# Kernel optimization log

Hardware: AMD Instinct MI355X
Metric: run time of the kernel (lower is better)

Reference implementation:

```python
import jax, jax.numpy as jnp
import numpy as np
from jax import lax

T, B, H, L = 512, 64, 512, 2  # seq_len, batch, hidden(=input), num_layers


def setup_inputs() -> dict:
    key = jax.random.key(0)
    ks = jax.random.split(key, 6)
    s = 1.0 / np.sqrt(H)  # torch default init scale
    x = jax.random.normal(ks[0], (T, B, H), dtype=jnp.float32)
    h0 = jax.random.normal(ks[1], (L, B, H), dtype=jnp.float32)
    W_ih = jax.random.uniform(ks[2], (L, H, H), jnp.float32, -s, s)
    W_hh = jax.random.uniform(ks[3], (L, H, H), jnp.float32, -s, s)
    b_ih = jax.random.uniform(ks[4], (L, H), jnp.float32, -s, s)
    b_hh = jax.random.uniform(ks[5], (L, H), jnp.float32, -s, s)
    return {"x": x, "h0": h0, "W_ih": W_ih, "W_hh": W_hh, "b_ih": b_ih, "b_hh": b_hh}


def _run_layer(x, h0, Wi, Wh, bi, bh):
    # Precompute input contribution for all timesteps: [T,B,H]
    xw = jnp.einsum('tbi,hi->tbh', x, Wi) + bi

    def step(h, xw_t):
        h_new = jnp.tanh(xw_t + h @ Wh.T + bh)
        return h_new, h_new

    h_last, ys = lax.scan(step, h0, xw)
    return ys, h_last


def reference(x, h0, W_ih, W_hh, b_ih, b_hh):
    # Multi-layer Elman RNN with tanh, matching torch.nn.RNN (batch_first=False).
    h_n = []
    out = x
    for l in range(L):
        out, h_last = _run_layer(out, h0[l], W_ih[l], W_hh[l], b_ih[l], b_hh[l])
        h_n.append(h_last)
    return out, jnp.stack(h_n, axis=0)
```

## Files before the change

kernel.cpp:

```cpp
#include <hip/hip_runtime.h>
#include <stdint.h>

#define T_ 512
#define B_ 64
#define H_ 512
#define L_ 2
#define TBH (T_*B_*H_)
#define BH  (B_*H_)
#define NC  8
#define CS  64
#define CROWS (CS*B_)
#define CSZ ((size_t)CROWS*H_)
#define WPK_OFF ((size_t)4*CSZ)
#define WPK_U4L (64*512)

typedef float    f32x4 __attribute__((ext_vector_type(4)));
typedef short    s16x8 __attribute__((ext_vector_type(8)));
typedef short    s16x4 __attribute__((ext_vector_type(4)));
typedef _Float16 h2    __attribute__((ext_vector_type(2)));

static __device__ __forceinline__ short f2bf(float f) {
  uint32_t u = __float_as_uint(f);
  u = (u + 0x7fffu + ((u >> 16) & 1u)) >> 16;
  return (short)u;
}

static __device__ __forceinline__ float fdot2(h2 a, h2 b, float c) {
#if __has_builtin(__builtin_amdgcn_fdot2)
  return __builtin_amdgcn_fdot2(a, b, c, false);
#else
  return c + (float)a[0] * (float)b[0] + (float)a[1] * (float)b[1];
#endif
}

template <int IMM>
static __device__ __forceinline__ float swz(float v) {
  return __int_as_float(__builtin_amdgcn_ds_swizzle(__float_as_int(v), IMM));
}

static __device__ __forceinline__ float dpp_xor1(float v) {
  return __int_as_float(__builtin_amdgcn_mov_dpp(__float_as_int(v), 0xB1, 0xF, 0xF, true));
}
static __device__ __forceinline__ float dpp_xor2(float v) {
  return __int_as_float(__builtin_amdgcn_mov_dpp(__float_as_int(v), 0x4E, 0xF, 0xF, true));
}

static __device__ __forceinline__ void rawbar() {
  __builtin_amdgcn_sched_barrier(0);
  asm volatile("s_waitcnt lgkmcnt(0)" ::: "memory");
  __builtin_amdgcn_s_barrier();
  __builtin_amdgcn_sched_barrier(0);
}

static __device__ __forceinline__ uint32_t pack2(float a, float b) {
  h2 p = { (_Float16)a, (_Float16)b };
  return __builtin_bit_cast(uint32_t, p);
}

static __device__ __forceinline__ h2 bch(uint32_t u) {
  return __builtin_bit_cast(h2, u);
}

__global__ __launch_bounds__(512, 1)
void prepack(const float* __restrict__ Whh, float* __restrict__ ws) {
  const int l = blockIdx.x;
  const int tid = threadIdx.x;
  const int c = tid & 7, rg = tid >> 3;
  uint4* dst = (uint4*)(ws + WPK_OFF) + (size_t)l * WPK_U4L;
  const float* W = Whh + (size_t)l * H_ * H_;
  #pragma unroll
  for (int k = 0; k < 8; ++k) {
    const float* wrow = W + (size_t)(rg * 8 + k) * H_ + c * 64;
    #pragma unroll
    for (int u = 0; u < 6; ++u) {
      f32x4 w4 = *(const f32x4*)(wrow + u * 8);
      f32x4 w5 = *(const f32x4*)(wrow + u * 8 + 4);
      uint4 pk;
      pk.x = pack2(w4.x, w4.y);
      pk.y = pack2(w4.z, w4.w);
      pk.z = pack2(w5.x, w5.y);
      pk.w = pack2(w5.z, w5.w);
      dst[(k * 6 + u) * 512 + tid] = pk;
    }
    #pragma unroll
    for (int p = 0; p < 2; ++p) {
      f32x4 w4 = *(const f32x4*)(wrow + 48 + p * 8);
      f32x4 w5 = *(const f32x4*)(wrow + 48 + p * 8 + 4);
      uint4 pk;
      pk.x = pack2(w4.x, w4.y);
      pk.y = pack2(w4.z, w4.w);
      pk.z = pack2(w5.x, w5.y);
      pk.w = pack2(w5.z, w5.w);
      dst[(48 + k * 2 + p) * 512 + tid] = pk;
    }
  }
}

__device__ void gemm_role(char* smem, int rb,
                          const float* __restrict__ In,
                          const float* __restrict__ W,
                          const float* __restrict__ bi,
                          const float* __restrict__ bh,
                          float* __restrict__ Out) {
  constexpr int LDT = 40;
  short* As = (short*)smem;
  short* Bs = (short*)(smem + 256 * LDT * 2);

  const int tid  = threadIdx.x;
  const int m0   = (rb >> 2) * 256;
  const int n0   = (rb & 3) * 128;
  const int wave = tid >> 6, lane = tid & 63;
  const int wm   = (wave >> 1) * 64;
  const int wn   = (wave & 1) * 64;
  const int quad = lane >> 4, tq = lane & 15;

  f32x4 acc[4][4] = {};

  for (int k0 = 0; k0 < 512; k0 += 32) {
    #pragma unroll
    for (int v = 0; v < 4; ++v) {
      int idx = v * 512 + tid;
      int r = idx >> 3, cc = (idx & 7) * 4;
      f32x4 a = *(const f32x4*)(In + (size_t)(m0 + r) * 512 + k0 + cc);
      s16x4 ap = { f2bf(a.x), f2bf(a.y), f2bf(a.z), f2bf(a.w) };
      *(s16x4*)(&As[r * LDT + cc]) = ap;
    }
    #pragma unroll
    for (int v = 0; v < 2; ++v) {
      int idx = v * 512 + tid;
      int r = idx >> 3, cc = (idx & 7) * 4;
      f32x4 b = *(const f32x4*)(W + (size_t)(n0 + r) * 512 + k0 + cc);
      s16x4 bp = { f2bf(b.x), f2bf(b.y), f2bf(b.z), f2bf(b.w) };
      *(s16x4*)(&Bs[r * LDT + cc]) = bp;
    }
    __syncthreads();

    s16x8 af[4], bfr[4];
    #pragma unroll
    for (int mf = 0; mf < 4; ++mf)
      af[mf] = *(const s16x8*)(&As[(wm + mf * 16 + tq) * LDT + quad * 8]);
    #pragma unroll
    for (int nf = 0; nf < 4; ++nf)
      bfr[nf] = *(const s16x8*)(&Bs[(wn + nf * 16 + tq) * LDT + quad * 8]);
    #pragma unroll
    for (int mf = 0; mf < 4; ++mf)
      #pragma unroll
      for (int nf = 0; nf < 4; ++nf)
        acc[mf][nf] = __builtin_amdgcn_mfma_f32_16x16x32_bf16(
            af[mf], bfr[nf], acc[mf][nf], 0, 0, 0);
    __syncthreads();
  }

  #pragma unroll
  for (int nf = 0; nf < 4; ++nf) {
    int col = n0 + wn + nf * 16 + tq;
    float bv = bi[col] + bh[col];
    #pragma unroll
    for (int mf = 0; mf < 4; ++mf) {
      #pragma unroll
      for (int r = 0; r < 4; ++r) {
        int row = m0 + wm + mf * 16 + quad * 4 + r;
        Out[(size_t)row * 512 + col] = acc[mf][nf][r] + bv;
      }
    }
  }
}

__device__ void recur_role(char* smem, int b, int chunk,
                           float* __restrict__ xw_y,
                           const float* __restrict__ h0l,
                           const uint4* __restrict__ wpk,
                           float* __restrict__ hstate) {
  const int tid = threadIdx.x;
  const int c   = tid & 7;

  uint4*    wlds = (uint4*)smem;
  _Float16* hbuf = (_Float16*)(smem + 131072);

  const uint4* wp = wpk + tid;
  h2 wreg[8][24];
  #pragma unroll
  for (int k = 0; k < 8; ++k)
    #pragma unroll
    for (int u = 0; u < 6; ++u) {
      uint4 v = wp[(k * 6 + u) * 512];
      wreg[k][u * 4 + 0] = bch(v.x);
      wreg[k][u * 4 + 1] = bch(v.y);
      wreg[k][u * 4 + 2] = bch(v.z);
      wreg[k][u * 4 + 3] = bch(v.w);
    }
  #pragma unroll
  for (int j = 0; j < 16; ++j)
    wlds[j * 512 + tid] = wp[(48 + j) * 512];

  float hini = (chunk == 0) ? h0l[b * 512 + tid] : hstate[b * 512 + tid];
  hbuf[(tid >> 6) * 72 + (tid & 63)] = (_Float16)hini;
  __syncthreads();

#define UBLK(HV, W0)                                                        \
  { h2 p0 = bch((HV).x), p1 = bch((HV).y), p2 = bch((HV).z), p3 = bch((HV).w); \
    _Pragma("unroll")                                                       \
    for (int k = 0; k < 8; ++k) {                                           \
      acc[k] = fdot2(wreg[k][(W0) + 0], p0, acc[k]);                        \
      acc[k] = fdot2(wreg[k][(W0) + 1], p1, acc[k]);                        \
      acc[k] = fdot2(wreg[k][(W0) + 2], p2, acc[k]);                        \
      acc[k] = fdot2(wreg[k][(W0) + 3], p3, acc[k]);                        \
    } }

#define WLDX(g)                                                             \
  { wt0 = wlds[(4 * (g) + 0) * 512 + tid];                                  \
    wt1 = wlds[(4 * (g) + 1) * 512 + tid];                                  \
    wt2 = wlds[(4 * (g) + 2) * 512 + tid];                                  \
    wt3 = wlds[(4 * (g) + 3) * 512 + tid]; }

#define CONSX(K0)                                                           \
  { h2 q0 = bch(q4.x), q1 = bch(q4.y), q2 = bch(q4.z), q3 = bch(q4.w);      \
    h2 r0 = bch(r4.x), r1 = bch(r4.y), r2 = bch(r4.z), r3 = bch(r4.w);      \
    float a = acc[(K0)];                                                    \
    a = fdot2(bch(wt0.x), q0, a); a = fdot2(bch(wt0.y), q1, a);             \
    a = fdot2(bch(wt0.z), q2, a); a = fdot2(bch(wt0.w), q3, a);             \
    a = fdot2(bch(wt1.x), r0, a); a = fdot2(bch(wt1.y), r1, a);             \
    a = fdot2(bch(wt1.z), r2, a); a = fdot2(bch(wt1.w), r3, a);             \
    acc[(K0)] = a;                                                          \
    a = acc[(K0) + 1];                                                      \
    a = fdot2(bch(wt2.x), q0, a); a = fdot2(bch(wt2.y), q1, a);             \
    a = fdot2(bch(wt2.z), q2, a); a = fdot2(bch(wt2.w), q3, a);             \
    a = fdot2(bch(wt3.x), r0, a); a = fdot2(bch(wt3.y), r1, a);             \
    a = fdot2(bch(wt3.z), r2, a); a = fdot2(bch(wt3.w), r3, a);             \
    acc[(K0) + 1] = a; }

  const float* xwp = xw_y + (size_t)b * 512 + tid;
  float xwv = xwp[0];
  float hlast = 0.f;
  for (int ls = 0; ls < CS; ++ls) {
    const int cur = ls & 1, nxt = cur ^ 1;
    int tn = (ls + 1 < CS) ? ls + 1 : ls;
    float xwn = xwp[(size_t)tn * BH];

    const _Float16* hc = &hbuf[cur * 8 * 72 + c * 72];
#define HLD(i) (*(const uint4*)(hc + (i) * 8))

    float acc[8] = {0, 0, 0, 0, 0, 0, 0, 0};

    uint4 ha = HLD(0), hbv = HLD(1), hx = HLD(2);
    uint4 q4 = HLD(6), r4 = HLD(7);
    uint4 wt0, wt1, wt2, wt3;

    WLDX(0);
    UBLK(ha, 0);   ha  = HLD(3);
    CONSX(0);      WLDX(1);
    UBLK(hbv, 4);  hbv = HLD(4);
    CONSX(2);      WLDX(2);
    UBLK(hx, 8);   hx  = HLD(5);
    CONSX(4);      WLDX(3);
    UBLK(ha, 12);
    CONSX(6);
    UBLK(hbv, 16);
    UBLK(hx, 20);

    float r1v[4];
    #pragma unroll
    for (int p = 0; p < 4; ++p) {
      float send = (c & 1) ? acc[2 * p] : acc[2 * p + 1];
      float recv = dpp_xor1(send);
      float keep = (c & 1) ? acc[2 * p + 1] : acc[2 * p];
      r1v[p] = keep + recv;
    }
    float r2v[2];
    #pragma unroll
    for (int p = 0; p < 2; ++p) {
      float send = (c & 2) ? r1v[2 * p] : r1v[2 * p + 1];
      float recv = dpp_xor2(send);
      float keep = (c & 2) ? r1v[2 * p + 1] : r1v[2 * p];
      r2v[p] = keep + recv;
    }
    {
      float send = (c & 4) ? r2v[0] : r2v[1];
      float recv = swz<0x101F>(send);
      float keep = (c & 4) ? r2v[1] : r2v[0];
      float dot  = keep + recv;

      float pre = dot + xwv;
      float e   = __expf(2.f * pre);
      float hni = 1.f - 2.f / (e + 1.f);
      hbuf[nxt * 8 * 72 + (tid >> 6) * 72 + (tid & 63)] = (_Float16)hni;
      xw_y[(size_t)ls * BH + b * 512 + tid] = hni;
      hlast = hni;
    }
    rawbar();
    xwv = xwn;
#undef HLD
  }
  hstate[b * 512 + tid] = hlast;
#undef UBLK
#undef WLDX
#undef CONSX
}

__global__ __launch_bounds__(512, 1)
void stage(int s,
           const float* __restrict__ x, const float* __restrict__ h0,
           const float* __restrict__ Wih, const float* __restrict__ Whh,
           const float* __restrict__ bih, const float* __restrict__ bhh,
           float* __restrict__ ws, float* __restrict__ out) {
  __shared__ __align__(16) char smem[133376];
  const int role = blockIdx.x >> 6;
  const int rb   = blockIdx.x & 63;
  float* hn = out + (size_t)TBH;
  const uint4* wpk = (const uint4*)(ws + WPK_OFF);

  if (role == 0) {
    int cc = s;
    if (cc < 0 || cc >= NC) return;
    recur_role(smem, rb, cc, ws + (size_t)(cc & 3) * CSZ, h0, wpk, hn);
  } else if (role == 1) {
    int cc = s - 2;
    if (cc < 0 || cc >= NC) return;
    recur_role(smem, rb, cc, out + (size_t)cc * CSZ, h0 + BH,
               wpk + WPK_U4L, hn + BH);
  } else if (role == 2) {
    int cc = s + 1;
    if (cc < 0 || cc >= NC) return;
    gemm_role(smem, rb, x + (size_t)cc * CSZ, Wih, bih, bhh,
              ws + (size_t)(cc & 3) * CSZ);
  } else {
    int cc = s - 1;
    if (cc < 0 || cc >= NC) return;
    gemm_role(smem, rb, ws + (size_t)(cc & 3) * CSZ,
              Wih + (size_t)H_ * H_, bih + H_, bhh + H_,
              out + (size_t)cc * CSZ);
  }
}

extern "C" void kernel_launch(void* const* d_in, const int* in_sizes, int n_in,
                              void* d_out, int out_size, void* d_ws, size_t ws_size,
                              hipStream_t stream) {
  const float* x   = (const float*)d_in[0];
  const float* h0  = (const float*)d_in[1];
  const float* Wih = (const float*)d_in[2];
  const float* Whh = (const float*)d_in[3];
  const float* bih = (const float*)d_in[4];
  const float* bhh = (const float*)d_in[5];
  float* out = (float*)d_out;
  float* ws  = (float*)d_ws;

  prepack<<<2, 512, 0, stream>>>(Whh, ws);
  for (int s = -1; s <= NC + 1; ++s)
    stage<<<256, 512, 0, stream>>>(s, x, h0, Wih, Whh, bih, bhh, ws, out);
}
```

Before: 1.248 ms.

## Replace per-stage kernel launches with persistent kernel using atomic counter sync

Folds the eleven wavefront-stage launches into one persistent kernel of 224 workgroups. Each role loops over chunks and hands off to the next through global atomic counters with spin-waits, instead of relying on kernel boundaries. Recurrent workgroups load their packed weights into registers and LDS once rather than once per chunk, and keep the hidden state on chip between chunks. The layer-2 GEMM uses 32 workgroups that each handle two tiles. The design depends on all 224 workgroups being resident at the same time, since otherwise the spin-waits could deadlock, and it adds spin-wait and fence overhead.

```diff
diff --git a/kernel.cpp b/kernel.cpp
--- a/kernel.cpp
+++ b/kernel.cpp
@@ -13,6 +13,8 @@
 #define CSZ ((size_t)CROWS*H_)
 #define WPK_OFF ((size_t)4*CSZ)
 #define WPK_U4L (64*512)
+#define CNT_OFF (WPK_OFF + (size_t)2*WPK_U4L*4)
+#define NWG 224
 
 typedef float    f32x4 __attribute__((ext_vector_type(4)));
 typedef short    s16x8 __attribute__((ext_vector_type(8)));
@@ -59,6 +61,22 @@
 
 static __device__ __forceinline__ h2 bch(uint32_t u) {
   return __builtin_bit_cast(h2, u);
+}
+
+static __device__ __forceinline__ void arrive(uint32_t* c) {
+  __syncthreads();
+  __threadfence();
+  if (threadIdx.x == 0)
+    __hip_atomic_fetch_add(c, 1u, __ATOMIC_RELEASE, __HIP_MEMORY_SCOPE_AGENT);
+}
+static __device__ __forceinline__ void waitg(uint32_t* c, uint32_t tgt) {
+  if (threadIdx.x == 0) {
+    while (__hip_atomic_load(c, __ATOMIC_RELAXED, __HIP_MEMORY_SCOPE_AGENT) < tgt)
+      __builtin_amdgcn_s_sleep(16);
+    (void)__hip_atomic_load(c, __ATOMIC_ACQUIRE, __HIP_MEMORY_SCOPE_AGENT);
+  }
+  __syncthreads();
+  __threadfence();
 }
 
 __global__ __launch_bounds__(512, 1)
@@ -166,19 +184,12 @@
   }
 }
 
-__device__ void recur_role(char* smem, int b, int chunk,
-                           float* __restrict__ xw_y,
-                           const float* __restrict__ h0l,
-                           const uint4* __restrict__ wpk,
-                           float* __restrict__ hstate) {
+static __device__ __forceinline__ void load_pack(char* smem,
+                                                 const uint4* __restrict__ wpk,
+                                                 h2 (&wreg)[8][24]) {
   const int tid = threadIdx.x;
-  const int c   = tid & 7;
-
-  uint4*    wlds = (uint4*)smem;
-  _Float16* hbuf = (_Float16*)(smem + 131072);
-
+  uint4* wlds = (uint4*)smem;
   const uint4* wp = wpk + tid;
-  h2 wreg[8][24];
   #pragma unroll
   for (int k = 0; k < 8; ++k)
     #pragma unroll
@@ -192,10 +203,22 @@
   #pragma unroll
   for (int j = 0; j < 16; ++j)
     wlds[j * 512 + tid] = wp[(48 + j) * 512];
-
-  float hini = (chunk == 0) ? h0l[b * 512 + tid] : hstate[b * 512 + tid];
-  hbuf[(tid >> 6) * 72 + (tid & 63)] = (_Float16)hini;
-  __syncthreads();
+}
+
+static __device__ float run_chunk(char* smem, int b, int first,
+                                  h2 (&wreg)[8][24],
+                                  float* __restrict__ xw_y,
+                                  const float* __restrict__ h0l) {
+  const int tid = threadIdx.x;
+  const int c   = tid & 7;
+  uint4*    wlds = (uint4*)smem;
+  _Float16* hbuf = (_Float16*)(smem + 131072);
+
+  if (first) {
+    float hini = h0l[b * 512 + tid];
+    hbuf[(tid >> 6) * 72 + (tid & 63)] = (_Float16)hini;
+    __syncthreads();
+  }
 
 #define UBLK(HV, W0)                                                        \
   { h2 p0 = bch((HV).x), p1 = bch((HV).y), p2 = bch((HV).z), p3 = bch((HV).w); \
@@ -291,44 +314,69 @@
     xwv = xwn;
 #undef HLD
   }
-  hstate[b * 512 + tid] = hlast;
+  return hlast;
 #undef UBLK
 #undef WLDX
 #undef CONSX
 }
 
 __global__ __launch_bounds__(512, 1)
-void stage(int s,
-           const float* __restrict__ x, const float* __restrict__ h0,
-           const float* __restrict__ Wih, const float* __restrict__ Whh,
-           const float* __restrict__ bih, const float* __restrict__ bhh,
-           float* __restrict__ ws, float* __restrict__ out) {
+void rnn_all(const float* __restrict__ x, const float* __restrict__ h0,
+             const float* __restrict__ Wih,
+             const float* __restrict__ bih, const float* __restrict__ bhh,
+             float* __restrict__ ws, float* __restrict__ out) {
   __shared__ __align__(16) char smem[133376];
-  const int role = blockIdx.x >> 6;
-  const int rb   = blockIdx.x & 63;
+  const int bid = blockIdx.x;
+  const int tid = threadIdx.x;
   float* hn = out + (size_t)TBH;
   const uint4* wpk = (const uint4*)(ws + WPK_OFF);
-
-  if (role == 0) {
-    int cc = s;
-    if (cc < 0 || cc >= NC) return;
-    recur_role(smem, rb, cc, ws + (size_t)(cc & 3) * CSZ, h0, wpk, hn);
-  } else if (role == 1) {
-    int cc = s - 2;
-    if (cc < 0 || cc >= NC) return;
-    recur_role(smem, rb, cc, out + (size_t)cc * CSZ, h0 + BH,
-               wpk + WPK_U4L, hn + BH);
-  } else if (role == 2) {
-    int cc = s + 1;
-    if (cc < 0 || cc >= NC) return;
-    gemm_role(smem, rb, x + (size_t)cc * CSZ, Wih, bih, bhh,
-              ws + (size_t)(cc & 3) * CSZ);
+  uint32_t* cnt = (uint32_t*)(ws + CNT_OFF);
+  uint32_t* g1a = cnt;
+  uint32_t* c1a = cnt + 16;
+  uint32_t* c2a = cnt + 32;
+
+  if (bid < 64) {
+    const int b = bid;
+    h2 wreg[8][24];
+    load_pack(smem, wpk, wreg);
+    float hlast = 0.f;
+    for (int cc = 0; cc < NC; ++cc) {
+      waitg(&g1a[cc], 64u);
+      hlast = run_chunk(smem, b, cc == 0, wreg,
+                        ws + (size_t)(cc & 3) * CSZ, h0);
+      arrive(&c1a[cc]);
+    }
+    hn[b * 512 + tid] = hlast;
+  } else if (bid < 128) {
+    const int b = bid - 64;
+    h2 wreg[8][24];
+    load_pack(smem, wpk + WPK_U4L, wreg);
+    float hlast = 0.f;
+    for (int cc = 0; cc < NC; ++cc) {
+      waitg(&c2a[cc], 32u);
+      hlast = run_chunk(smem, b, cc == 0, wreg,
+                        out + (size_t)cc * CSZ, h0 + BH);
+    }
+    hn[BH + b * 512 + tid] = hlast;
+  } else if (bid < 192) {
+    const int rb = bid - 128;
+    for (int cc = 0; cc < NC; ++cc) {
+      if (cc >= 4) waitg(&c2a[cc - 4], 32u);
+      gemm_role(smem, rb, x + (size_t)cc * CSZ, Wih, bih, bhh,
+                ws + (size_t)(cc & 3) * CSZ);
+      arrive(&g1a[cc]);
+    }
   } else {
-    int cc = s - 1;
-    if (cc < 0 || cc >= NC) return;
-    gemm_role(smem, rb, ws + (size_t)(cc & 3) * CSZ,
-              Wih + (size_t)H_ * H_, bih + H_, bhh + H_,
-              out + (size_t)cc * CSZ);
+    const int g = bid - 192;
+    const float* W2  = Wih + (size_t)H_ * H_;
+    for (int cc = 0; cc < NC; ++cc) {
+      waitg(&c1a[cc], 64u);
+      gemm_role(smem, 2 * g,     ws + (size_t)(cc & 3) * CSZ, W2,
+                bih + H_, bhh + H_, out + (size_t)cc * CSZ);
+      gemm_role(smem, 2 * g + 1, ws + (size_t)(cc & 3) * CSZ, W2,
+                bih + H_, bhh + H_, out + (size_t)cc * CSZ);
+      arrive(&c2a[cc]);
+    }
   }
 }
 
@@ -344,7 +392,7 @@
   float* out = (float*)d_out;
   float* ws  = (float*)d_ws;
 
+  hipMemsetAsync((char*)d_ws + CNT_OFF * sizeof(float), 0, 512, stream);
   prepack<<<2, 512, 0, stream>>>(Whh, ws);
-  for (int s = -1; s <= NC + 1; ++s)
-    stage<<<256, 512, 0, stream>>>(s, x, h0, Wih, Whh, bih, bhh, ws, out);
-}
+  rnn_all<<<NWG, 512, 0, stream>>>(x, h0, Wih, bih, bhh, ws, out);
+}
```

Result: slower. 1.408 ms (+12.8%).

## Pre-convert GEMM operands to bf16 once and store layer-1 output as bf16

Applied to the files above, without the earlier changes.

A wider prepack kernel converts W_ih and the whole input x to bf16 up front, staging x in the first half of each output chunk. Layer-0 recurrence also writes its hidden outputs as a separate bf16 copy that the layer-1 GEMM reads. The input-projection GEMM then loads bf16 tiles straight into LDS with no per-tile fp32-to-bf16 conversion and half the global read bytes. The cost is an extra full pass over x before the pipeline, more workspace, and reuse of the output buffer as scratch, which depends on chunk ordering.

```diff
diff --git a/kernel.cpp b/kernel.cpp
--- a/kernel.cpp
+++ b/kernel.cpp
@@ -11,8 +11,11 @@
 #define CS  64
 #define CROWS (CS*B_)
 #define CSZ ((size_t)CROWS*H_)
-#define WPK_OFF ((size_t)4*CSZ)
-#define WPK_U4L (64*512)
+#define WPK_OFF  ((size_t)4*CSZ)
+#define WPK_U4L  (64*512)
+#define WIHP_OFF (WPK_OFF + (size_t)2*WPK_U4L*4)
+#define Y1_OFF   (WIHP_OFF + (size_t)262144)
+#define Y1SZ     ((size_t)CROWS*H_)
 
 typedef float    f32x4 __attribute__((ext_vector_type(4)));
 typedef short    s16x8 __attribute__((ext_vector_type(8)));
@@ -62,43 +65,71 @@
 }
 
 __global__ __launch_bounds__(512, 1)
-void prepack(const float* __restrict__ Whh, float* __restrict__ ws) {
-  const int l = blockIdx.x;
-  const int tid = threadIdx.x;
-  const int c = tid & 7, rg = tid >> 3;
-  uint4* dst = (uint4*)(ws + WPK_OFF) + (size_t)l * WPK_U4L;
-  const float* W = Whh + (size_t)l * H_ * H_;
-  #pragma unroll
-  for (int k = 0; k < 8; ++k) {
-    const float* wrow = W + (size_t)(rg * 8 + k) * H_ + c * 64;
-    #pragma unroll
-    for (int u = 0; u < 6; ++u) {
-      f32x4 w4 = *(const f32x4*)(wrow + u * 8);
-      f32x4 w5 = *(const f32x4*)(wrow + u * 8 + 4);
-      uint4 pk;
-      pk.x = pack2(w4.x, w4.y);
-      pk.y = pack2(w4.z, w4.w);
-      pk.z = pack2(w5.x, w5.y);
-      pk.w = pack2(w5.z, w5.w);
-      dst[(k * 6 + u) * 512 + tid] = pk;
-    }
-    #pragma unroll
-    for (int p = 0; p < 2; ++p) {
-      f32x4 w4 = *(const f32x4*)(wrow + 48 + p * 8);
-      f32x4 w5 = *(const f32x4*)(wrow + 48 + p * 8 + 4);
-      uint4 pk;
-      pk.x = pack2(w4.x, w4.y);
-      pk.y = pack2(w4.z, w4.w);
-      pk.z = pack2(w5.x, w5.y);
-      pk.w = pack2(w5.z, w5.w);
-      dst[(48 + k * 2 + p) * 512 + tid] = pk;
+void prepack(const float* __restrict__ Whh, const float* __restrict__ Wih,
+             const float* __restrict__ x, float* __restrict__ ws,
+             float* __restrict__ out) {
+  const int bid = blockIdx.x, tid = threadIdx.x;
+  if (bid < 2) {
+    const int l = bid, c = tid & 7, rg = tid >> 3;
+    uint4* dst = (uint4*)(ws + WPK_OFF) + (size_t)l * WPK_U4L;
+    const float* W = Whh + (size_t)l * H_ * H_;
+    #pragma unroll
+    for (int k = 0; k < 8; ++k) {
+      const float* wrow = W + (size_t)(rg * 8 + k) * H_ + c * 64;
+      #pragma unroll
+      for (int u = 0; u < 6; ++u) {
+        f32x4 w4 = *(const f32x4*)(wrow + u * 8);
+        f32x4 w5 = *(const f32x4*)(wrow + u * 8 + 4);
+        uint4 pk;
+        pk.x = pack2(w4.x, w4.y);
+        pk.y = pack2(w4.z, w4.w);
+        pk.z = pack2(w5.x, w5.y);
+        pk.w = pack2(w5.z, w5.w);
+        dst[(k * 6 + u) * 512 + tid] = pk;
+      }
+      #pragma unroll
+      for (int p = 0; p < 2; ++p) {
+        f32x4 w4 = *(const f32x4*)(wrow + 48 + p * 8);
+        f32x4 w5 = *(const f32x4*)(wrow + 48 + p * 8 + 4);
+        uint4 pk;
+        pk.x = pack2(w4.x, w4.y);
+        pk.y = pack2(w4.z, w4.w);
+        pk.z = pack2(w5.x, w5.y);
+        pk.w = pack2(w5.z, w5.w);
+        dst[(48 + k * 2 + p) * 512 + tid] = pk;
+      }
+    }
+  } else if (bid < 4) {
+    const int l = bid - 2;
+    const float* src = Wih + (size_t)l * H_ * H_;
+    short* dst = (short*)(ws + WIHP_OFF) + (size_t)l * H_ * H_;
+    for (int it = 0; it < 64; ++it) {
+      int e = (it * 512 + tid) * 8;
+      f32x4 a = *(const f32x4*)(src + e);
+      f32x4 b = *(const f32x4*)(src + e + 4);
+      s16x8 p = { f2bf(a.x), f2bf(a.y), f2bf(a.z), f2bf(a.w),
+                  f2bf(b.x), f2bf(b.y), f2bf(b.z), f2bf(b.w) };
+      *(s16x8*)(dst + e) = p;
+    }
+  } else {
+    const int w = bid - 4;
+    const int cc = w >> 3, sub = w & 7;
+    const float* src = x + (size_t)cc * CSZ + (size_t)sub * (CSZ / 8);
+    short* dst = (short*)(out + (size_t)cc * CSZ) + (size_t)sub * (CSZ / 8);
+    for (int it = 0; it < 64; ++it) {
+      int e = (it * 512 + tid) * 8;
+      f32x4 a = *(const f32x4*)(src + e);
+      f32x4 b = *(const f32x4*)(src + e + 4);
+      s16x8 p = { f2bf(a.x), f2bf(a.y), f2bf(a.z), f2bf(a.w),
+                  f2bf(b.x), f2bf(b.y), f2bf(b.z), f2bf(b.w) };
+      *(s16x8*)(dst + e) = p;
     }
   }
 }
 
 __device__ void gemm_role(char* smem, int rb,
-                          const float* __restrict__ In,
-                          const float* __restrict__ W,
+                          const short* __restrict__ In,
+                          const short* __restrict__ W,
                           const float* __restrict__ bi,
                           const float* __restrict__ bh,
                           float* __restrict__ Out) {
@@ -118,20 +149,16 @@
 
   for (int k0 = 0; k0 < 512; k0 += 32) {
     #pragma unroll
-    for (int v = 0; v < 4; ++v) {
-      int idx = v * 512 + tid;
-      int r = idx >> 3, cc = (idx & 7) * 4;
-      f32x4 a = *(const f32x4*)(In + (size_t)(m0 + r) * 512 + k0 + cc);
-      s16x4 ap = { f2bf(a.x), f2bf(a.y), f2bf(a.z), f2bf(a.w) };
-      *(s16x4*)(&As[r * LDT + cc]) = ap;
-    }
-    #pragma unroll
     for (int v = 0; v < 2; ++v) {
       int idx = v * 512 + tid;
-      int r = idx >> 3, cc = (idx & 7) * 4;
-      f32x4 b = *(const f32x4*)(W + (size_t)(n0 + r) * 512 + k0 + cc);
-      s16x4 bp = { f2bf(b.x), f2bf(b.y), f2bf(b.z), f2bf(b.w) };
-      *(s16x4*)(&Bs[r * LDT + cc]) = bp;
+      int r = idx >> 2, cc = (idx & 3) * 8;
+      s16x8 a = *(const s16x8*)(In + (size_t)(m0 + r) * 512 + k0 + cc);
+      *(s16x8*)(&As[r * LDT + cc]) = a;
+    }
+    {
+      int r = tid >> 2, cc = (tid & 3) * 8;
+      s16x8 b = *(const s16x8*)(W + (size_t)(n0 + r) * 512 + k0 + cc);
+      *(s16x8*)(&Bs[r * LDT + cc]) = b;
     }
     __syncthreads();
 
@@ -166,8 +193,10 @@
   }
 }
 
+template <bool BF16Y>
 __device__ void recur_role(char* smem, int b, int chunk,
                            float* __restrict__ xw_y,
+                           short* __restrict__ yb,
                            const float* __restrict__ h0l,
                            const uint4* __restrict__ wpk,
                            float* __restrict__ hstate) {
@@ -284,7 +313,10 @@
       float e   = __expf(2.f * pre);
       float hni = 1.f - 2.f / (e + 1.f);
       hbuf[nxt * 8 * 72 + (tid >> 6) * 72 + (tid & 63)] = (_Float16)hni;
-      xw_y[(size_t)ls * BH + b * 512 + tid] = hni;
+      if constexpr (BF16Y)
+        yb[(size_t)ls * BH + b * 512 + tid] = f2bf(hni);
+      else
+        xw_y[(size_t)ls * BH + b * 512 + tid] = hni;
       hlast = hni;
     }
     rawbar();
@@ -298,36 +330,37 @@
 }
 
 __global__ __launch_bounds__(512, 1)
-void stage(int s,
-           const float* __restrict__ x, const float* __restrict__ h0,
-           const float* __restrict__ Wih, const float* __restrict__ Whh,
+void stage(int s, const float* __restrict__ h0,
            const float* __restrict__ bih, const float* __restrict__ bhh,
            float* __restrict__ ws, float* __restrict__ out) {
   __shared__ __align__(16) char smem[133376];
   const int role = blockIdx.x >> 6;
   const int rb   = blockIdx.x & 63;
   float* hn = out + (size_t)TBH;
-  const uint4* wpk = (const uint4*)(ws + WPK_OFF);
+  const uint4* wpk  = (const uint4*)(ws + WPK_OFF);
+  const short* wihp = (const short*)(ws + WIHP_OFF);
+  short*       y1b  = (short*)(ws + Y1_OFF);
 
   if (role == 0) {
     int cc = s;
     if (cc < 0 || cc >= NC) return;
-    recur_role(smem, rb, cc, ws + (size_t)(cc & 3) * CSZ, h0, wpk, hn);
+    recur_role<true>(smem, rb, cc, ws + (size_t)(cc & 3) * CSZ,
+                     y1b + (size_t)(cc & 3) * Y1SZ, h0, wpk, hn);
   } else if (role == 1) {
     int cc = s - 2;
     if (cc < 0 || cc >= NC) return;
-    recur_role(smem, rb, cc, out + (size_t)cc * CSZ, h0 + BH,
-               wpk + WPK_U4L, hn + BH);
+    recur_role<false>(smem, rb, cc, out + (size_t)cc * CSZ, nullptr,
+                      h0 + BH, wpk + WPK_U4L, hn + BH);
   } else if (role == 2) {
     int cc = s + 1;
     if (cc < 0 || cc >= NC) return;
-    gemm_role(smem, rb, x + (size_t)cc * CSZ, Wih, bih, bhh,
-              ws + (size_t)(cc & 3) * CSZ);
+    gemm_role(smem, rb, (const short*)(out + (size_t)cc * CSZ), wihp,
+              bih, bhh, ws + (size_t)(cc & 3) * CSZ);
   } else {
     int cc = s - 1;
     if (cc < 0 || cc >= NC) return;
-    gemm_role(smem, rb, ws + (size_t)(cc & 3) * CSZ,
-              Wih + (size_t)H_ * H_, bih + H_, bhh + H_,
+    gemm_role(smem, rb, y1b + (size_t)(cc & 3) * Y1SZ,
+              wihp + (size_t)H_ * H_, bih + H_, bhh + H_,
               out + (size_t)cc * CSZ);
   }
 }
@@ -344,7 +377,7 @@
   float* out = (float*)d_out;
   float* ws  = (float*)d_ws;
 
-  prepack<<<2, 512, 0, stream>>>(Whh, ws);
+  prepack<<<68, 512, 0, stream>>>(Whh, Wih, x, ws, out);
   for (int s = -1; s <= NC + 1; ++s)
-    stage<<<256, 512, 0, stream>>>(s, x, h0, Wih, Whh, bih, bhh, ws, out);
-}
+    stage<<<256, 512, 0, stream>>>(s, h0, bih, bhh, ws, out);
+}
```

Result: faster. 1.119 ms (median of 2 runs) (-10.4%).
